# Kernel tuning notes

Hardware: AMD Instinct MI355X
Metric: run time of the kernel (lower is better)

Reference implementation:

```python
import jax, jax.numpy as jnp
import numpy as np
from jax import lax

NUM_HEADS = 6
LN_EPS = 1e-5


def _ln(x, g, b):
    mu = jnp.mean(x, axis=-1, keepdims=True)
    var = jnp.mean(jnp.square(x - mu), axis=-1, keepdims=True)
    return (x - mu) * jax.lax.rsqrt(var + LN_EPS) * g + b


def _gelu(x):
    return jax.nn.gelu(x, approximate=False)


def setup_inputs() -> dict:
    key = jax.random.key(0)
    ks = jax.random.split(key, 16)
    B, N, C = 16, 1025, 384
    hid = 4 * C  # 1536
    k3 = 3  # depthwise kernel size
    s = 0.02
    rn = lambda k, shape: (jax.random.normal(k, shape, jnp.float32) * s)
    return {
        "x": jax.random.normal(ks[0], (B, N, C), jnp.float32),
        "ln1_g": jnp.ones((C,), jnp.float32),
        "ln1_b": jnp.zeros((C,), jnp.float32),
        "qkv_w": rn(ks[1], (3 * C, C)),
        "proj_w": rn(ks[2], (C, C)),
        "proj_b": jnp.zeros((C,), jnp.float32),
        "ln2_g": jnp.ones((C,), jnp.float32),
        "ln2_b": jnp.zeros((C,), jnp.float32),
        "conv1_w": rn(ks[3], (hid, C)),          # 1x1 conv as matrix
        "conv1_b": jnp.zeros((hid,), jnp.float32),
        "conv2_w": rn(ks[4], (hid, 1, k3, k3)),   # depthwise OIHW
        "conv2_b": jnp.zeros((hid,), jnp.float32),
        "conv3_w": rn(ks[5], (C, hid)),           # 1x1 conv as matrix
        "conv3_b": jnp.zeros((C,), jnp.float32),
        "bn1_s": jnp.ones((hid,), jnp.float32), "bn1_b": jnp.zeros((hid,), jnp.float32),
        "bn2_s": jnp.ones((hid,), jnp.float32), "bn2_b": jnp.zeros((hid,), jnp.float32),
        "bn3_s": jnp.ones((C,), jnp.float32), "bn3_b": jnp.zeros((C,), jnp.float32),
        "comp_w": rn(ks[6], (C // 4, C)), "comp_b": jnp.zeros((C // 4,), jnp.float32),
        "exc_w": rn(ks[7], (C, C // 4)), "exc_b": jnp.zeros((C,), jnp.float32),
    }


def _block(x, ln1_g, ln1_b, qkv_w, proj_w, proj_b, ln2_g, ln2_b,
           conv1_w, conv1_b, conv2_w, conv2_b, conv3_w, conv3_b,
           bn1_s, bn1_b, bn2_s, bn2_b, bn3_s, bn3_b,
           comp_w, comp_b, exc_w, exc_b):
    B, N, C = x.shape
    Hh = NUM_HEADS
    hd = C // Hh
    S = int(np.sqrt(N - 1))

    # ---- Attention (manual softmax(QK^T)V) ----
    h = _ln(x, ln1_g, ln1_b)
    qkv = jnp.einsum('bnc,dc->bnd', h, qkv_w).reshape(B, N, 3, Hh, hd)
    qkv = qkv.transpose(2, 0, 3, 1, 4)  # [3,B,H,N,hd]
    q, k, v = qkv[0], qkv[1], qkv[2]
    attn = jax.nn.softmax(jnp.einsum('bhqd,bhkd->bhqk', q, k) * (hd ** -0.5), axis=-1)
    o = jnp.einsum('bhqk,bhkd->bhqd', attn, v).transpose(0, 2, 1, 3).reshape(B, N, C)
    o = o @ proj_w.T + proj_b
    x = x + o

    # ---- DAFF FFN (conv + BN(eval affine) + GELU + SE gating on cls) ----
    h2 = _ln(x, ln2_g, ln2_b)
    cls_tok, tok = h2[:, :1], h2[:, 1:]
    t = tok.reshape(B, S, S, C).transpose(0, 3, 1, 2)  # NCHW
    hid = conv1_w.shape[0]
    y = jnp.einsum('bchw,oc->bohw', t, conv1_w) + conv1_b[None, :, None, None]
    y = y * bn1_s[None, :, None, None] + bn1_b[None, :, None, None]
    y = _gelu(y)
    shortcut = y
    y = lax.conv_general_dilated(y, conv2_w, (1, 1), 'SAME',
                                 feature_group_count=hid,
                                 dimension_numbers=('NCHW', 'OIHW', 'NCHW'))
    y = y + conv2_b[None, :, None, None]
    y = y * bn2_s[None, :, None, None] + bn2_b[None, :, None, None]
    y = shortcut + _gelu(y)
    y = jnp.einsum('bchw,oc->bohw', y, conv3_w) + conv3_b[None, :, None, None]
    y = y * bn3_s[None, :, None, None] + bn3_b[None, :, None, None]
    # SE gate on cls token
    w = jnp.mean(y, axis=(2, 3)).reshape(B, 1, C)
    w = _gelu(w @ comp_w.T + comp_b) @ exc_w.T + exc_b
    cls_out = cls_tok * w
    tok_out = y.reshape(B, C, S * S).transpose(0, 2, 1)
    out = jnp.concatenate([cls_out, tok_out], axis=1)
    return x + out


def reference(x, ln1_g, ln1_b, qkv_w, proj_w, proj_b, ln2_g, ln2_b,
              conv1_w, conv1_b, conv2_w, conv2_b, conv3_w, conv3_b,
              bn1_s, bn1_b, bn2_s, bn2_b, bn3_s, bn3_b,
              comp_w, comp_b, exc_w, exc_b):
    return _block(x, ln1_g, ln1_b, qkv_w, proj_w, proj_b, ln2_g, ln2_b,
                  conv1_w, conv1_b, conv2_w, conv2_b, conv3_w, conv3_b,
                  bn1_s, bn1_b, bn2_s, bn2_b, bn3_s, bn3_b,
                  comp_w, comp_b, exc_w, exc_b)
```

## Files before the change

kernel.cpp:

```cpp
#include <hip/hip_runtime.h>
#include <math.h>

#define DI __device__ __forceinline__

namespace {

constexpr int B_ = 16;
constexpr int N_ = 1025;
constexpr int C_ = 384;
constexpr int H_ = 6;
constexpr int HD_ = 64;
constexpr int HID_ = 1536;
constexpr int P_ = 1024;
constexpr int MTOK = B_ * P_;
constexpr int MALL = B_ * N_;
constexpr int NPAD = 1088;
constexpr long long AF = (long long)MALL * C_;

constexpr int NQKV = 3 * C_ * C_;
constexpr int NPROJ = C_ * C_;
constexpr int NC1 = HID_ * C_;
constexpr int NC3 = C_ * HID_;
constexpr int NW2 = HID_ * 9;
constexpr int T1 = NQKV, T2 = T1 + NPROJ, T3 = T2 + NC1, T4 = T3 + NC3;
constexpr int T5 = T4 + NW2, T6 = T5 + HID_;

typedef __attribute__((ext_vector_type(4))) float f32x4;
typedef __attribute__((ext_vector_type(16))) float f32x16;
typedef __attribute__((ext_vector_type(8))) short bf16x8;

DI float gelu_f(float x) { return 0.5f * x * (1.0f + erff(x * 0.7071067811865475f)); }

DI float us2f(unsigned short u) {
  union { unsigned int i; float f; } c; c.i = ((unsigned)u) << 16; return c.f;
}
DI unsigned short f2us(float f) {
  union { float f; unsigned int i; } c; c.f = f;
  unsigned int r = c.i + 0x7FFF + ((c.i >> 16) & 1);
  return (unsigned short)(r >> 16);
}
DI unsigned short f2us_trunc(float f) {
  union { float f; unsigned int i; } c; c.f = f;
  return (unsigned short)(c.i >> 16);
}
DI void bf8_to_f(const uint4 v, float* f) {
  const unsigned int u[4] = {v.x, v.y, v.z, v.w};
#pragma unroll
  for (int t = 0; t < 4; t++) {
    union { unsigned int i; float fl; } lo, hi;
    lo.i = (u[t] & 0xffffu) << 16;
    hi.i = u[t] & 0xffff0000u;
    f[2 * t] = lo.fl; f[2 * t + 1] = hi.fl;
  }
}
DI uint4 f_to_bf8(const float* f) {
  unsigned int w[4];
#pragma unroll
  for (int t = 0; t < 4; t++)
    w[t] = (unsigned)f2us(f[2 * t]) | ((unsigned)f2us(f[2 * t + 1]) << 16);
  return make_uint4(w[0], w[1], w[2], w[3]);
}

DI unsigned cvt_pk_bf16(float lo, float hi) {
  unsigned d;
  asm("v_cvt_pk_bf16_f32 %0, %1, %2" : "=v"(d) : "v"(lo), "v"(hi));
  return d;
}
DI void permswap(unsigned &a, unsigned &b) {
  asm("v_permlane32_swap_b32 %0, %1" : "+v"(a), "+v"(b));
}

DI void gl2lds16(const unsigned short* g, unsigned short* l) {
  __builtin_amdgcn_global_load_lds(
      (const __attribute__((address_space(1))) void*)g,
      (__attribute__((address_space(3))) void*)l, 16, 0, 0);
}

__global__ __launch_bounds__(256) void cvtall_kernel(
    const float* __restrict__ qkv_w, const float* __restrict__ proj_w,
    const float* __restrict__ conv1_w, const float* __restrict__ conv3_w,
    const float* __restrict__ conv2_w, const float* __restrict__ c2b,
    const float* __restrict__ s2, const float* __restrict__ b2,
    unsigned short* __restrict__ dst16, float* __restrict__ Bc)
{
  const int idx = blockIdx.x * 256 + threadIdx.x;
  if (idx < T1)      dst16[idx] = f2us(qkv_w[idx]);
  else if (idx < T2) dst16[idx] = f2us(proj_w[idx - T1]);
  else if (idx < T3) dst16[idx] = f2us(conv1_w[idx - T2]);
  else if (idx < T4) dst16[idx] = f2us(conv3_w[idx - T3]);
  else if (idx < T5) {
    const int r = idx - T4, tap = r / HID_, c = r % HID_;
    dst16[idx] = f2us(conv2_w[c * 9 + tap] * s2[c]);
  } else if (idx < T6) {
    const int c = idx - T5;
    Bc[c] = c2b[c] * s2[c] + b2[c];
  }
}

__global__ __launch_bounds__(256) void lnw_kernel(
    const float* __restrict__ x, const float* __restrict__ g,
    const float* __restrict__ b, unsigned short* __restrict__ out,
    float* __restrict__ cls_out, int nrows)
{
  const int row = blockIdx.x * 4 + (threadIdx.x >> 6);
  if (row >= nrows) return;
  const int lane = threadIdx.x & 63;
  const float* xr = x + (long long)row * C_;
  float v[6];
#pragma unroll
  for (int i = 0; i < 6; i++) v[i] = xr[lane + 64 * i];
  float s = 0.f, q = 0.f;
#pragma unroll
  for (int i = 0; i < 6; i++) { s += v[i]; q += v[i] * v[i]; }
#pragma unroll
  for (int m = 1; m < 64; m <<= 1) {
    s += __shfl_xor(s, m, 64);
    q += __shfl_xor(q, m, 64);
  }
  const float mean = s * (1.0f / C_);
  const float var  = q * (1.0f / C_) - mean * mean;
  const float rstd = rsqrtf(var + 1e-5f);
  unsigned short* orow = out + (long long)row * C_;
  const bool iscls = (cls_out != nullptr) && (row % N_) == 0;
  float* cr = iscls ? cls_out + (long long)(row / N_) * C_ : nullptr;
#pragma unroll
  for (int i = 0; i < 6; i++) {
    const int c = lane + 64 * i;
    const float r = (v[i] - mean) * rstd * g[c] + b[c];
    orow[c] = f2us(r);
    if (iscls) cr[c] = r;
  }
}

__global__ __launch_bounds__(256) void vtrans_kernel(
    const unsigned short* __restrict__ v, unsigned short* __restrict__ vt)
{
  __shared__ unsigned short t[64][72];
  const int bh = blockIdx.x, nt = blockIdx.y;
  const int n0 = nt * 64;
  const int tid = threadIdx.x;
  {
    const int nl = tid >> 2;
    const int dc = (tid & 3) * 16;
    const int gn = n0 + nl;
    uint4 a = make_uint4(0u,0u,0u,0u), b = make_uint4(0u,0u,0u,0u);
    if (gn < N_) {
      const unsigned short* p = v + ((long long)bh * N_ + gn) * HD_ + dc;
      a = *(const uint4*)p; b = *(const uint4*)(p + 8);
    }
    *(uint4*)&t[nl][dc] = a;
    *(uint4*)&t[nl][dc + 8] = b;
  }
  __syncthreads();
  {
    const int dl = tid >> 2;
    const int nc = (tid & 3) * 16;
    unsigned short tmp[16];
#pragma unroll
    for (int i = 0; i < 16; i++) tmp[i] = t[nc + i][dl];
    unsigned short* p = vt + ((long long)bh * HD_ + dl) * NPAD + n0 + nc;
    *(uint4*)p = *(uint4*)&tmp[0];
    *(uint4*)(p + 8) = *(uint4*)&tmp[8];
  }
}

enum { GM_QKV = 0, GM_PROJ = 1, GM_CONV1 = 2, GM_CONV3 = 3 };

template <int MODE, int K>
__global__ __launch_bounds__(256) void mgemm_kernel(
    const unsigned short* __restrict__ A, const unsigned short* __restrict__ W,
    void* __restrict__ o0, void* __restrict__ o1, void* __restrict__ o2,
    const float* __restrict__ e0, const float* __restrict__ e1,
    const float* __restrict__ e2, int M)
{
  __shared__ unsigned short As[128][64];
  __shared__ unsigned short Bs[128][64];
  const int m0 = blockIdx.x * 128, n0 = blockIdx.y * 128;
  if (m0 >= M) return;
  const int tid = threadIdx.x;
  const int lane = tid & 63, wv = tid >> 6;
  const int lane15 = lane & 15, quad = lane >> 4;
  const int wm = (wv >> 1) * 64, wn = (wv & 1) * 64;

  const unsigned short* agp[4];
  const unsigned short* bgp[4];
#pragma unroll
  for (int t = 0; t < 4; t++) {
    const int lr = wv * 32 + t * 8 + (lane >> 3);
    const int chunk = (lane & 7) ^ (lr & 7);
    int gm = m0 + lr;
    if (gm > M - 1) gm = M - 1;
    long long arow = gm;
    if constexpr (MODE == GM_CONV1) arow = (long long)(gm >> 10) * N_ + 1 + (gm & 1023);
    agp[t] = A + arow * K + chunk * 8;
    bgp[t] = W + (long long)(n0 + lr) * K + chunk * 8;
  }

  f32x4 acc[4][4];
#pragma unroll
  for (int i = 0; i < 4; i++)
#pragma unroll
    for (int j = 0; j < 4; j++) acc[i][j] = (f32x4)0.f;

  const int xsel = lane15 & 7;
  for (int k0 = 0; k0 < K; k0 += 64) {
    __syncthreads();
#pragma unroll
    for (int t = 0; t < 4; t++) {
      gl2lds16(agp[t] + k0, &As[wv * 32 + t * 8][0]);
      gl2lds16(bgp[t] + k0, &Bs[wv * 32 + t * 8][0]);
    }
    __syncthreads();
#pragma unroll
    for (int kh = 0; kh < 2; kh++) {
      bf16x8 af[4], bfr[4];
#pragma unroll
      for (int i = 0; i < 4; i++)
        af[i] = *(const bf16x8*)&As[wm + i * 16 + lane15][((kh * 4 + quad) ^ xsel) * 8];
#pragma unroll
      for (int j = 0; j < 4; j++)
        bfr[j] = *(const bf16x8*)&Bs[wn + j * 16 + lane15][((kh * 4 + quad) ^ xsel) * 8];
#pragma unroll
      for (int i = 0; i < 4; i++)
#pragma unroll
        for (int j = 0; j < 4; j++)
          acc[i][j] = __builtin_amdgcn_mfma_f32_16x16x32_bf16(af[i], bfr[j], acc[i][j], 0, 0, 0);
    }
  }
#pragma unroll
  for (int i = 0; i < 4; i++) {
#pragma unroll
    for (int r = 0; r < 4; r++) {
      const int m = m0 + wm + i * 16 + quad * 4 + r;
      if (m >= M) continue;
#pragma unroll
      for (int j = 0; j < 4; j++) {
        const int n = n0 + wn + j * 16 + lane15;
        const float val = acc[i][j][r];
        if constexpr (MODE == GM_QKV) {
          const int which = n / C_, rr = n % C_, hh = rr >> 6, e = rr & 63;
          const int b = m / N_, nn = m % N_;
          unsigned short* dst = (unsigned short*)((which == 0) ? o0 : ((which == 1) ? o1 : o2));
          const float sval = (which == 0) ? val * 0.18033688f : val;
          dst[(((long long)b * H_ + hh) * N_ + nn) * HD_ + e] = f2us(sval);
        } else if constexpr (MODE == GM_PROJ) {
          ((float*)o0)[(long long)m * C_ + n] = val + e0[(long long)m * C_ + n] + e1[n];
        } else if constexpr (MODE == GM_CONV1) {
          ((unsigned short*)o0)[(long long)m * HID_ + n] =
              f2us(gelu_f((val + e0[n]) * e1[n] + e2[n]));
        } else {
          const float val2 = (val + e0[n]) * e1[n] + e2[n];
          ((float*)o0)[(long long)m * C_ + n] = val2;
          const int bb = m >> 10, pp = m & 1023;
          const long long orow = ((long long)bb * N_ + 1 + pp) * C_ + n;
          ((float*)o1)[orow] = ((const float*)o2)[orow] + val2;
        }
      }
    }
  }
}

__global__ __launch_bounds__(256) void fattn_kernel(
    const unsigned short* __restrict__ q, const unsigned short* __restrict__ k,
    const unsigned short* __restrict__ vt, unsigned short* __restrict__ o)
{
  __shared__ unsigned short Ks[2][64][64];
  __shared__ unsigned short Vt[2][64][64];
  const int tid = threadIdx.x;
  const int lane = tid & 63, wv = tid >> 6;
  const int lane31 = lane & 31, half = lane >> 5;
  const int x7 = lane & 7;
  const int bh = blockIdx.x, qt = blockIdx.y;
  const long long headoff = (long long)bh * N_;
  const int q0w = qt * 128 + wv * 32;
  const bool active = q0w < N_;

  int gq = q0w + lane31; if (gq > N_ - 1) gq = N_ - 1;
  const unsigned short* qp = q + (headoff + gq) * HD_ + half * 8;
  bf16x8 qf[4];
#pragma unroll
  for (int m = 0; m < 4; m++) qf[m] = *(const bf16x8*)(qp + m * 16);

  const unsigned short* kgp[2];
  const unsigned short* vgp[2];
#pragma unroll
  for (int t = 0; t < 2; t++) {
    const int r = t * 32 + wv * 8 + (lane >> 3);
    const int ch = (lane & 7) ^ (r & 7);
    kgp[t] = k + (headoff + r) * HD_ + ch * 8;
    vgp[t] = vt + ((long long)bh * HD_ + r) * NPAD + ch * 8;
  }

  f32x16 O0 = (f32x16)0.f, O1 = (f32x16)0.f;
  float l = 0.f;

#pragma unroll
  for (int t = 0; t < 2; t++) {
    gl2lds16(kgp[t], &Ks[0][t * 32 + wv * 8][0]);
    gl2lds16(vgp[t], &Vt[0][t * 32 + wv * 8][0]);
  }
  __syncthreads();

  for (int kt = 0; kt < 17; kt++) {
    const int cur = kt & 1;
    if (kt < 16) {
      const long long koff = (long long)(kt + 1) * 64;
#pragma unroll
      for (int t = 0; t < 2; t++) {
        gl2lds16(kgp[t] + koff * HD_, &Ks[cur ^ 1][t * 32 + wv * 8][0]);
        gl2lds16(vgp[t] + koff, &Vt[cur ^ 1][t * 32 + wv * 8][0]);
      }
    }
    if (active) {
      f32x16 S0 = (f32x16)0.f, S1 = (f32x16)0.f;
      __builtin_amdgcn_s_setprio(1);
#pragma unroll
      for (int m = 0; m < 4; m++) {
        const int chs = ((m * 2 + half) ^ x7) * 8;
        const bf16x8 k0 = *(const bf16x8*)&Ks[cur][lane31][chs];
        const bf16x8 k1 = *(const bf16x8*)&Ks[cur][32 + lane31][chs];
        S0 = __builtin_amdgcn_mfma_f32_32x32x16_bf16(k0, qf[m], S0, 0, 0, 0);
        S1 = __builtin_amdgcn_mfma_f32_32x32x16_bf16(k1, qf[m], S1, 0, 0, 0);
      }
      __builtin_amdgcn_s_setprio(0);
      if (kt == 16) {
#pragma unroll
        for (int r = 0; r < 16; r++) {
          const int kl = (r & 3) + 8 * (r >> 2) + 4 * half;
          if (1024 + kl >= N_) S0[r] = -1e30f;
          S1[r] = -1e30f;
        }
      }
      unsigned pk0[8], pk1[8];
#pragma unroll
      for (int s = 0; s < 8; s++) {
        const float a0 = exp2f(S0[2 * s]), a1 = exp2f(S0[2 * s + 1]);
        const float b0 = exp2f(S1[2 * s]), b1 = exp2f(S1[2 * s + 1]);
        l += (a0 + a1) + (b0 + b1);
        pk0[s] = cvt_pk_bf16(a0, a1);
        pk1[s] = cvt_pk_bf16(b0, b1);
      }
      unsigned wkc[4][4];
#pragma unroll
      for (int bb = 0; bb < 2; bb++) {
#pragma unroll
        for (int kc2 = 0; kc2 < 2; kc2++) {
          unsigned a0 = bb ? pk1[kc2 * 4 + 0] : pk0[kc2 * 4 + 0];
          unsigned a2 = bb ? pk1[kc2 * 4 + 2] : pk0[kc2 * 4 + 2];
          permswap(a0, a2);
          unsigned a1 = bb ? pk1[kc2 * 4 + 1] : pk0[kc2 * 4 + 1];
          unsigned a3 = bb ? pk1[kc2 * 4 + 3] : pk0[kc2 * 4 + 3];
          permswap(a1, a3);
          const int kc = bb * 2 + kc2;
          wkc[kc][0] = a0; wkc[kc][1] = a1; wkc[kc][2] = a2; wkc[kc][3] = a3;
        }
      }
      __builtin_amdgcn_s_setprio(1);
#pragma unroll
      for (int kc = 0; kc < 4; kc++) {
        union { unsigned u[4]; bf16x8 v; } pa;
        pa.u[0] = wkc[kc][0]; pa.u[1] = wkc[kc][1];
        pa.u[2] = wkc[kc][2]; pa.u[3] = wkc[kc][3];
        const int chv = ((kc * 2 + half) ^ x7) * 8;
        const bf16x8 v0 = *(const bf16x8*)&Vt[cur][lane31][chv];
        const bf16x8 v1 = *(const bf16x8*)&Vt[cur][32 + lane31][chv];
        O0 = __builtin_amdgcn_mfma_f32_32x32x16_bf16(pa.v, v0, O0, 0, 0, 0);
        O1 = __builtin_amdgcn_mfma_f32_32x32x16_bf16(pa.v, v1, O1, 0, 0, 0);
      }
      __builtin_amdgcn_s_setprio(0);
    }
    __syncthreads();
  }

  l += __shfl_xor(l, 32, 64);
  const float rinv = 1.0f / l;
  float li[16];
#pragma unroll
  for (int r = 0; r < 16; r++) {
    const int qloc = (r & 3) + 8 * (r >> 2) + 4 * half;
    li[r] = __int_as_float(
        __builtin_amdgcn_ds_bpermute(qloc * 4, __float_as_int(rinv)));
  }
  const int b = bh / H_, hh = bh % H_;
#pragma unroll
  for (int r = 0; r < 16; r++) {
    const int qloc = (r & 3) + 8 * (r >> 2) + 4 * half;
    const int gqr = q0w + qloc;
    if (gqr < N_) {
      const long long orow = ((long long)b * N_ + gqr) * C_ + hh * HD_;
      o[orow + lane31] = f2us(O0[r] * li[r]);
      o[orow + 32 + lane31] = f2us(O1[r] * li[r]);
    }
  }
}

__global__ __launch_bounds__(192) void dwconv_kernel(
    const unsigned short* __restrict__ y1, const unsigned short* __restrict__ w2s,
    const float* __restrict__ Bc, unsigned short* __restrict__ y2)
{
  const int jp = blockIdx.x & 15;
  const int i  = (blockIdx.x >> 4) & 31;
  const int b  = blockIdx.x >> 9;
  const int j0 = jp * 2;
  const int cb = threadIdx.x << 3;

  float wf[9][8];
#pragma unroll
  for (int tap = 0; tap < 9; tap++) {
    const uint4 wv = *(const uint4*)(w2s + tap * HID_ + cb);
    bf8_to_f(wv, wf[tap]);
  }
  float acc0[8] = {}, acc1[8] = {};
  float sh0[8], sh1[8];
#pragma unroll
  for (int di = -1; di <= 1; di++) {
    const int ii = i + di;
    if (ii < 0 || ii > 31) continue;
    const long long rowbase = ((long long)b * P_ + ii * 32) * HID_ + cb;
#pragma unroll
    for (int dj = -1; dj <= 2; dj++) {
      const int jj = j0 + dj;
      if (jj < 0 || jj > 31) continue;
      const uint4 dv = *(const uint4*)(y1 + rowbase + (long long)jj * HID_);
      float df[8]; bf8_to_f(dv, df);
      if (dj <= 1) {
        const int tap = (di + 1) * 3 + (dj + 1);
#pragma unroll
        for (int t = 0; t < 8; t++) acc0[t] += df[t] * wf[tap][t];
      }
      if (dj >= 0) {
        const int tap = (di + 1) * 3 + dj;
#pragma unroll
        for (int t = 0; t < 8; t++) acc1[t] += df[t] * wf[tap][t];
      }
      if (di == 0 && dj == 0) {
#pragma unroll
        for (int t = 0; t < 8; t++) sh0[t] = df[t];
      }
      if (di == 0 && dj == 1) {
#pragma unroll
        for (int t = 0; t < 8; t++) sh1[t] = df[t];
      }
    }
  }
  const float4 bc0 = *(const float4*)(Bc + cb);
  const float4 bc1 = *(const float4*)(Bc + cb + 4);
  const float bcv[8] = {bc0.x, bc0.y, bc0.z, bc0.w, bc1.x, bc1.y, bc1.z, bc1.w};
  float of0[8], of1[8];
#pragma unroll
  for (int t = 0; t < 8; t++) {
    of0[t] = sh0[t] + gelu_f(acc0[t] + bcv[t]);
    of1[t] = sh1[t] + gelu_f(acc1[t] + bcv[t]);
  }
  const long long tok0 = ((long long)b * P_ + i * 32 + j0) * HID_ + cb;
  *(uint4*)(y2 + tok0) = f_to_bf8(of0);
  *(uint4*)(y2 + tok0 + HID_) = f_to_bf8(of1);
}

__global__ __launch_bounds__(384) void pool_kernel(const float* __restrict__ y3,
                                                   float* __restrict__ w0p)
{
  const int b = blockIdx.x, chunk = blockIdx.y;
  const int c = threadIdx.x;
  float s = 0.f;
  for (int p = chunk * 64; p < chunk * 64 + 64; p++)
    s += y3[((long long)b * P_ + p) * C_ + c];
  w0p[((long long)b * 16 + chunk) * C_ + c] = s;
}

__global__ __launch_bounds__(128) void se_kernel(
    const float* __restrict__ w0p, const float* __restrict__ cw,
    const float* __restrict__ cb, const float* __restrict__ ew,
    const float* __restrict__ eb, float* __restrict__ wfin)
{
  __shared__ float wm[384];
  __shared__ float t1[96];
  const int b = blockIdx.x, t = threadIdx.x;
  for (int c = t; c < 384; c += 128) {
    float s = 0.f;
    for (int ch = 0; ch < 16; ch++) s += w0p[((long long)b * 16 + ch) * C_ + c];
    wm[c] = s * (1.0f / 1024.0f);
  }
  __syncthreads();
  if (t < 96) {
    float s = cb[t];
    for (int c = 0; c < 384; c++) s += wm[c] * cw[t * 384 + c];
    t1[t] = gelu_f(s);
  }
  __syncthreads();
  for (int c = t; c < 384; c += 128) {
    float s = eb[c];
    for (int j = 0; j < 96; j++) s += t1[j] * ew[c * 96 + j];
    wfin[(long long)b * C_ + c] = s;
  }
}

__global__ __launch_bounds__(256) void clsfix_kernel(
    const float* __restrict__ x2, const float* __restrict__ cls,
    const float* __restrict__ wfin, float* __restrict__ out)
{
  const int idx = blockIdx.x * 256 + threadIdx.x;
  if (idx >= B_ * C_) return;
  const int b = idx / C_, c = idx % C_;
  const long long row = (long long)b * N_ * C_ + c;
  out[row] = x2[row] + cls[idx] * wfin[idx];
}

}

extern "C" void kernel_launch(void* const* d_in, const int* in_sizes, int n_in,
                              void* d_out, int out_size, void* d_ws, size_t ws_size,
                              hipStream_t stream)
{
  const float* x       = (const float*)d_in[0];
  const float* ln1_g   = (const float*)d_in[1];
  const float* ln1_b   = (const float*)d_in[2];
  const float* qkv_w   = (const float*)d_in[3];
  const float* proj_w  = (const float*)d_in[4];
  const float* proj_b  = (const float*)d_in[5];
  const float* ln2_g   = (const float*)d_in[6];
  const float* ln2_b   = (const float*)d_in[7];
  const float* conv1_w = (const float*)d_in[8];
  const float* conv1_b = (const float*)d_in[9];
  const float* conv2_w = (const float*)d_in[10];
  const float* conv2_b = (const float*)d_in[11];
  const float* conv3_w = (const float*)d_in[12];
  const float* conv3_b = (const float*)d_in[13];
  const float* bn1_s   = (const float*)d_in[14];
  const float* bn1_b   = (const float*)d_in[15];
  const float* bn2_s   = (const float*)d_in[16];
  const float* bn2_b   = (const float*)d_in[17];
  const float* bn3_s   = (const float*)d_in[18];
  const float* bn3_b   = (const float*)d_in[19];
  const float* comp_w  = (const float*)d_in[20];
  const float* comp_b  = (const float*)d_in[21];
  const float* exc_w   = (const float*)d_in[22];
  const float* exc_b   = (const float*)d_in[23];

  char* wsb = (char*)d_ws;
  const size_t RA = 50331648, RB = 50331648, RC = 25190400;
  const size_t tailbytes = (size_t)T5 * 2 +
                           (size_t)(HID_ + B_ * C_ + B_ * 16 * C_ + B_ * C_) * 4;
  const size_t needed = RA + RB + RC + tailbytes;
  if (ws_size < needed) return;

  unsigned short* qb  = (unsigned short*)wsb;
  unsigned short* kb  = qb + AF;
  unsigned short* vb  = kb + AF;
  unsigned short* h2b = (unsigned short*)wsb;
  unsigned short* y2  = (unsigned short*)wsb;
  char* rb = wsb + RA;
  unsigned short* hb  = (unsigned short*)rb;
  unsigned short* o16 = (unsigned short*)rb;
  unsigned short* y1  = (unsigned short*)rb;
  float* y3           = (float*)rb;
  unsigned short* vtb = (unsigned short*)(wsb + RA + RB);
  float* x2 = (float*)(wsb + RA + RB);
  unsigned short* w16 = (unsigned short*)(wsb + RA + RB + RC);
  unsigned short* wqkv16  = w16;
  unsigned short* wproj16 = w16 + T1;
  unsigned short* wc116   = w16 + T2;
  unsigned short* wc316   = w16 + T3;
  unsigned short* w2s     = w16 + T4;
  float* Bc   = (float*)(w16 + T5);
  float* cls  = Bc + HID_;
  float* w0p  = cls + B_ * C_;
  float* wfin = w0p + B_ * 16 * C_;

  cvtall_kernel<<<(T6 + 255) / 256, 256, 0, stream>>>(
      qkv_w, proj_w, conv1_w, conv3_w, conv2_w, conv2_b, bn2_s, bn2_b, w16, Bc);
  lnw_kernel<<<(MALL + 3) / 4, 256, 0, stream>>>(x, ln1_g, ln1_b, hb, nullptr, MALL);
  mgemm_kernel<GM_QKV, 384><<<dim3(136, 9), 256, 0, stream>>>(
      hb, wqkv16, qb, kb, vb, nullptr, nullptr, nullptr, MALL);
  vtrans_kernel<<<dim3(B_ * H_, 17), 256, 0, stream>>>(vb, vtb);
  fattn_kernel<<<dim3(B_ * H_, 9), 256, 0, stream>>>(qb, kb, vtb, o16);
  mgemm_kernel<GM_PROJ, 384><<<dim3(136, 3), 256, 0, stream>>>(
      o16, wproj16, x2, nullptr, nullptr, x, proj_b, nullptr, MALL);
  lnw_kernel<<<(MALL + 3) / 4, 256, 0, stream>>>(x2, ln2_g, ln2_b, h2b, cls, MALL);
  mgemm_kernel<GM_CONV1, 384><<<dim3(128, 12), 256, 0, stream>>>(
      h2b, wc116, y1, nullptr, nullptr, conv1_b, bn1_s, bn1_b, MTOK);
  dwconv_kernel<<<B_ * 32 * 16, 192, 0, stream>>>(y1, w2s, Bc, y2);
  mgemm_kernel<GM_CONV3, 1536><<<dim3(128, 3), 256, 0, stream>>>(
      y2, wc316, y3, (float*)d_out, x2, conv3_b, bn3_s, bn3_b, MTOK);
  pool_kernel<<<dim3(B_, 16), 384, 0, stream>>>(y3, w0p);
  se_kernel<<<B_, 128, 0, stream>>>(w0p, comp_w, comp_b, exc_w, exc_b, wfin);
  clsfix_kernel<<<(B_ * C_ + 255) / 256, 256, 0, stream>>>(x2, cls, wfin, (float*)d_out);
}
```

Measured before the change: 417.7 us.

## Split attention key range across two wave groups and merge partial outputs

```diff
diff --git a/kernel.cpp b/kernel.cpp
--- a/kernel.cpp
+++ b/kernel.cpp
@@ -260,20 +260,25 @@
   }
 }
 
-__global__ __launch_bounds__(256) void fattn_kernel(
+__global__ __launch_bounds__(512) void fattn_kernel(
     const unsigned short* __restrict__ q, const unsigned short* __restrict__ k,
     const unsigned short* __restrict__ vt, unsigned short* __restrict__ o)
 {
-  __shared__ unsigned short Ks[2][64][64];
-  __shared__ unsigned short Vt[2][64][64];
+  __shared__ unsigned short smem[32768];
   const int tid = threadIdx.x;
   const int lane = tid & 63, wv = tid >> 6;
+  const int qw = wv & 3, kg = wv >> 2;
   const int lane31 = lane & 31, half = lane >> 5;
   const int x7 = lane & 7;
   const int bh = blockIdx.x, qt = blockIdx.y;
   const long long headoff = (long long)bh * N_;
-  const int q0w = qt * 128 + wv * 32;
+  const int q0w = qt * 128 + qw * 32;
   const bool active = q0w < N_;
+  const int nreal = kg ? 8 : 9;
+  const int kbase = kg * 576;
+
+  unsigned short* Ksm = smem;
+  unsigned short* Vsm = smem + 16384;
 
   int gq = q0w + lane31; if (gq > N_ - 1) gq = N_ - 1;
   const unsigned short* qp = q + (headoff + gq) * HD_ + half * 8;
@@ -285,10 +290,10 @@
   const unsigned short* vgp[2];
 #pragma unroll
   for (int t = 0; t < 2; t++) {
-    const int r = t * 32 + wv * 8 + (lane >> 3);
+    const int r = t * 32 + qw * 8 + (lane >> 3);
     const int ch = (lane & 7) ^ (r & 7);
-    kgp[t] = k + (headoff + r) * HD_ + ch * 8;
-    vgp[t] = vt + ((long long)bh * HD_ + r) * NPAD + ch * 8;
+    kgp[t] = k + (headoff + kbase + r) * HD_ + ch * 8;
+    vgp[t] = vt + ((long long)bh * HD_ + r) * NPAD + kbase + ch * 8;
   }
 
   f32x16 O0 = (f32x16)0.f, O1 = (f32x16)0.f;
@@ -296,34 +301,38 @@
 
 #pragma unroll
   for (int t = 0; t < 2; t++) {
-    gl2lds16(kgp[t], &Ks[0][t * 32 + wv * 8][0]);
-    gl2lds16(vgp[t], &Vt[0][t * 32 + wv * 8][0]);
+    gl2lds16(kgp[t], Ksm + (kg * 2 + 0) * 4096 + (t * 32 + qw * 8) * 64);
+    gl2lds16(vgp[t], Vsm + (kg * 2 + 0) * 4096 + (t * 32 + qw * 8) * 64);
   }
   __syncthreads();
 
-  for (int kt = 0; kt < 17; kt++) {
-    const int cur = kt & 1;
-    if (kt < 16) {
-      const long long koff = (long long)(kt + 1) * 64;
+  for (int it = 0; it < 9; it++) {
+    const int cur = it & 1;
+    if (it + 1 < nreal) {
+      const long long koff = (long long)(it + 1) * 64;
 #pragma unroll
       for (int t = 0; t < 2; t++) {
-        gl2lds16(kgp[t] + koff * HD_, &Ks[cur ^ 1][t * 32 + wv * 8][0]);
-        gl2lds16(vgp[t] + koff, &Vt[cur ^ 1][t * 32 + wv * 8][0]);
-      }
-    }
-    if (active) {
+        gl2lds16(kgp[t] + koff * HD_,
+                 Ksm + (kg * 2 + (cur ^ 1)) * 4096 + (t * 32 + qw * 8) * 64);
+        gl2lds16(vgp[t] + koff,
+                 Vsm + (kg * 2 + (cur ^ 1)) * 4096 + (t * 32 + qw * 8) * 64);
+      }
+    }
+    if (active && it < nreal) {
+      const unsigned short* Kb = Ksm + (kg * 2 + cur) * 4096;
+      const unsigned short* Vb = Vsm + (kg * 2 + cur) * 4096;
       f32x16 S0 = (f32x16)0.f, S1 = (f32x16)0.f;
       __builtin_amdgcn_s_setprio(1);
 #pragma unroll
       for (int m = 0; m < 4; m++) {
         const int chs = ((m * 2 + half) ^ x7) * 8;
-        const bf16x8 k0 = *(const bf16x8*)&Ks[cur][lane31][chs];
-        const bf16x8 k1 = *(const bf16x8*)&Ks[cur][32 + lane31][chs];
+        const bf16x8 k0 = *(const bf16x8*)&Kb[lane31 * 64 + chs];
+        const bf16x8 k1 = *(const bf16x8*)&Kb[(32 + lane31) * 64 + chs];
         S0 = __builtin_amdgcn_mfma_f32_32x32x16_bf16(k0, qf[m], S0, 0, 0, 0);
         S1 = __builtin_amdgcn_mfma_f32_32x32x16_bf16(k1, qf[m], S1, 0, 0, 0);
       }
       __builtin_amdgcn_s_setprio(0);
-      if (kt == 16) {
+      if (kg == 1 && it == 7) {
 #pragma unroll
         for (int r = 0; r < 16; r++) {
           const int kl = (r & 3) + 8 * (r >> 2) + 4 * half;
@@ -362,8 +371,8 @@
         pa.u[0] = wkc[kc][0]; pa.u[1] = wkc[kc][1];
         pa.u[2] = wkc[kc][2]; pa.u[3] = wkc[kc][3];
         const int chv = ((kc * 2 + half) ^ x7) * 8;
-        const bf16x8 v0 = *(const bf16x8*)&Vt[cur][lane31][chv];
-        const bf16x8 v1 = *(const bf16x8*)&Vt[cur][32 + lane31][chv];
+        const bf16x8 v0 = *(const bf16x8*)&Vb[lane31 * 64 + chv];
+        const bf16x8 v1 = *(const bf16x8*)&Vb[(32 + lane31) * 64 + chv];
         O0 = __builtin_amdgcn_mfma_f32_32x32x16_bf16(pa.v, v0, O0, 0, 0, 0);
         O1 = __builtin_amdgcn_mfma_f32_32x32x16_bf16(pa.v, v1, O1, 0, 0, 0);
       }
@@ -372,24 +381,43 @@
     __syncthreads();
   }
 
-  l += __shfl_xor(l, 32, 64);
-  const float rinv = 1.0f / l;
-  float li[16];
-#pragma unroll
-  for (int r = 0; r < 16; r++) {
-    const int qloc = (r & 3) + 8 * (r >> 2) + 4 * half;
-    li[r] = __int_as_float(
-        __builtin_amdgcn_ds_bpermute(qloc * 4, __float_as_int(rinv)));
-  }
-  const int b = bh / H_, hh = bh % H_;
-#pragma unroll
-  for (int r = 0; r < 16; r++) {
-    const int qloc = (r & 3) + 8 * (r >> 2) + 4 * half;
-    const int gqr = q0w + qloc;
-    if (gqr < N_) {
-      const long long orow = ((long long)b * N_ + gqr) * C_ + hh * HD_;
-      o[orow + lane31] = f2us(O0[r] * li[r]);
-      o[orow + 32 + lane31] = f2us(O1[r] * li[r]);
+  float* mrg = (float*)smem;
+  if (kg == 1 && active) {
+    float* mq = mrg + qw * 33 * 64 + lane;
+#pragma unroll
+    for (int j = 0; j < 16; j++) mq[j * 64] = O0[j];
+#pragma unroll
+    for (int j = 0; j < 16; j++) mq[(16 + j) * 64] = O1[j];
+    mq[32 * 64] = l;
+  }
+  __syncthreads();
+  if (kg == 0 && active) {
+    float* mq = mrg + qw * 33 * 64 + lane;
+#pragma unroll
+    for (int j = 0; j < 16; j++) O0[j] += mq[j * 64];
+#pragma unroll
+    for (int j = 0; j < 16; j++) O1[j] += mq[(16 + j) * 64];
+    l += mq[32 * 64];
+
+    l += __shfl_xor(l, 32, 64);
+    const float rinv = 1.0f / l;
+    float li[16];
+#pragma unroll
+    for (int r = 0; r < 16; r++) {
+      const int qloc = (r & 3) + 8 * (r >> 2) + 4 * half;
+      li[r] = __int_as_float(
+          __builtin_amdgcn_ds_bpermute(qloc * 4, __float_as_int(rinv)));
+    }
+    const int b = bh / H_, hh = bh % H_;
+#pragma unroll
+    for (int r = 0; r < 16; r++) {
+      const int qloc = (r & 3) + 8 * (r >> 2) + 4 * half;
+      const int gqr = q0w + qloc;
+      if (gqr < N_) {
+        const long long orow = ((long long)b * N_ + gqr) * C_ + hh * HD_;
+        o[orow + lane31] = f2us(O0[r] * li[r]);
+        o[orow + 32 + lane31] = f2us(O1[r] * li[r]);
+      }
     }
   }
 }
@@ -573,7 +601,7 @@
   mgemm_kernel<GM_QKV, 384><<<dim3(136, 9), 256, 0, stream>>>(
       hb, wqkv16, qb, kb, vb, nullptr, nullptr, nullptr, MALL);
   vtrans_kernel<<<dim3(B_ * H_, 17), 256, 0, stream>>>(vb, vtb);
-  fattn_kernel<<<dim3(B_ * H_, 9), 256, 0, stream>>>(qb, kb, vtb, o16);
+  fattn_kernel<<<dim3(B_ * H_, 9), 512, 0, stream>>>(qb, kb, vtb, o16);
   mgemm_kernel<GM_PROJ, 384><<<dim3(136, 3), 256, 0, stream>>>(
       o16, wproj16, x2, nullptr, nullptr, x, proj_b, nullptr, MALL);
   lnw_kernel<<<(MALL + 3) / 4, 256, 0, stream>>>(x2, ln2_g, ln2_b, h2b, cls, MALL);
```

Measured after the change: 414.6 us. No clear change (-0.7%).
